# Kernel tuning notes

Hardware: AMD Instinct MI355X
Metric: run time of the kernel (lower is better)

The kernel has to match this reference:

```python
import jax, jax.numpy as jnp
import numpy as np

B, K1, N, DIMS = 512, 11, 5, 784  # K1 = K+1 samples per class incl. query
H = 512  # model_size


def _lstm(x_seq, W, U, b):
    """Keras-style LSTM, return_sequences=True.
    x_seq: [B, T, I]; W: [I, 4H]; U: [H, 4H]; b: [4H]. Gate order i,f,g,o.
    """
    units = U.shape[0]
    bsz = x_seq.shape[0]
    # precompute input projections for all timesteps: [T, B, 4H]
    xw = jnp.einsum('bti,ih->tbh', x_seq, W) + b

    def step(carry, xw_t):
        h, c = carry
        z = xw_t + h @ U  # [B, 4H]
        i, f, g, o = jnp.split(z, 4, axis=-1)
        i = jax.nn.sigmoid(i)
        f = jax.nn.sigmoid(f)
        g = jnp.tanh(g)
        o = jax.nn.sigmoid(o)
        c = f * c + i * g
        h = o * jnp.tanh(c)
        return (h, c), h

    init = (jnp.zeros((bsz, units), x_seq.dtype), jnp.zeros((bsz, units), x_seq.dtype))
    _, hs = jax.lax.scan(step, init, xw)  # hs: [T, B, H]
    return jnp.transpose(hs, (1, 0, 2))  # [B, T, H]


def setup_inputs() -> dict:
    key = jax.random.key(0)
    ks = jax.random.split(key, 8)
    return {
        'input_images': jax.random.normal(ks[0], (B, K1, N, DIMS), jnp.float32),
        'input_labels': jax.random.uniform(ks[1], (B, K1, N, N), jnp.float32),
        'W1': jax.random.normal(ks[2], (N + DIMS, 4 * H), jnp.float32) * 0.02,
        'U1': jax.random.normal(ks[3], (H, 4 * H), jnp.float32) * 0.02,
        'b1': jnp.zeros((4 * H,), jnp.float32),
        'W2': jax.random.normal(ks[4], (H, 4 * N), jnp.float32) * 0.02,
        'U2': jax.random.normal(ks[5], (N, 4 * N), jnp.float32) * 0.02,
        'b2': jnp.zeros((4 * N,), jnp.float32),
    }


def reference(input_images, input_labels, W1, U1, b1, W2, U2, b2):
    K = K1 - 1
    support_imgs = input_images[:, :K]               # [B, K, N, D]
    query_imgs = input_images[:, -1].reshape(-1, 1, N, DIMS)  # [B, 1, N, D]
    support_lbls = input_labels[:, :K]               # [B, K, N, N]
    concat_support = jnp.concatenate([support_imgs, support_lbls], axis=-1)
    zero_lbls = jnp.zeros((B, 1, N, N), input_images.dtype)
    concat_query = jnp.concatenate([query_imgs, zero_lbls], axis=-1)
    seq = jnp.concatenate([concat_support, concat_query], axis=1)  # [B, K1, N, N+D]
    seq = seq.reshape(-1, N * K1, N + DIMS)          # [B, T, N+D], T = N*K1
    x = _lstm(seq, W1, U1, b1)                       # [B, T, H]
    out = _lstm(x, W2, U2, b2)                       # [B, T, N]
    return out.reshape(-1, K1, N, N)
```

## Files before the change

### kernel.cpp

```cpp
#include <hip/hip_runtime.h>

typedef __attribute__((ext_vector_type(8))) __bf16 bf16x8;
typedef __attribute__((ext_vector_type(8))) unsigned short ushort8;
typedef __attribute__((ext_vector_type(4))) float f32x4;
typedef __attribute__((ext_vector_type(2))) unsigned long long u64x2;

#define DEVINL __device__ __forceinline__
#define RLX __ATOMIC_RELAXED
#define AGT __HIP_MEMORY_SCOPE_AGENT

constexpr int B_C    = 512;
constexpr int DIMS_C = 784;
constexpr int T_C    = 55;
constexpr int I0_C   = 789;
constexpr int KP_C   = 800;
constexpr int H_C    = 512;
constexpr int G4_C   = 2048;
constexpr int M1_C   = 28160;

constexpr size_t OFF_A    = 0;
constexpr size_t SZ_A     = (size_t)M1_C * KP_C * 2;
constexpr size_t OFF_W1T  = OFF_A + SZ_A;
constexpr size_t SZ_W1T   = (size_t)G4_C * KP_C * 2;
constexpr size_t OFF_U1T  = OFF_W1T + SZ_W1T;
constexpr size_t SZ_U1T   = (size_t)G4_C * H_C * 2;
constexpr size_t OFF_XW1  = OFF_U1T + SZ_U1T;
constexpr size_t SZ_XW1   = (size_t)M1_C * G4_C * 2;
constexpr size_t OFF_H    = OFF_XW1 + SZ_XW1;
constexpr size_t SZ_H     = (size_t)2 * B_C * H_C * 2;
constexpr size_t OFF_XMID = OFF_H + SZ_H;
constexpr size_t SZ_XMID  = (size_t)M1_C * H_C * 4;
constexpr size_t OFF_XW2  = OFF_XMID + SZ_XMID;
constexpr size_t SZ_XW2   = (size_t)M1_C * 20 * 4;
constexpr size_t OFF_W2T  = OFF_XW2 + SZ_XW2;
constexpr size_t SZ_W2T   = (size_t)20 * H_C * 4;
constexpr size_t OFF_CNT  = OFF_W2T + SZ_W2T;

DEVINL unsigned short f2bf(float f) {
  unsigned u = __builtin_bit_cast(unsigned, f);
  u += 0x7fffu + ((u >> 16) & 1u);
  return (unsigned short)(u >> 16);
}
DEVINL float sigm(float x) {
  return __builtin_amdgcn_rcpf(1.f + __builtin_amdgcn_exp2f(-1.4426950408889634f * x));
}
DEVINL float tanh_(float x) {
  return 2.f * __builtin_amdgcn_rcpf(1.f + __builtin_amdgcn_exp2f(-2.8853900817779268f * x)) - 1.f;
}
DEVINL void gl_lds16(const void* g, void* l) {
  __builtin_amdgcn_global_load_lds((const __attribute__((address_space(1))) void*)g,
                                   (__attribute__((address_space(3))) void*)l, 16, 0, 0);
}
DEVINL void gl_lds16_coh(const void* g, void* l) {
  __builtin_amdgcn_global_load_lds((const __attribute__((address_space(1))) void*)g,
                                   (__attribute__((address_space(3))) void*)l, 16, 0, 17);
}


__global__ void pack_a(const float* __restrict__ img, const float* __restrict__ lbl,
                       unsigned short* __restrict__ A) {
  int gid = blockIdx.x * blockDim.x + threadIdx.x;
  constexpr int CPR = KP_C / 8;
  if (gid >= M1_C * CPR) return;
  int r  = gid / CPR;
  int cc = gid - r * CPR;
  int t = r >> 9, b = r & 511;
  int k1 = t / 5, n = t - k1 * 5;
  int c0 = cc * 8;
  ushort8 v;
  if (c0 + 8 <= DIMS_C) {
    const float* p = img + ((size_t)((b * 11 + k1) * 5 + n)) * DIMS_C + c0;
    f32x4 x0 = *(const f32x4*)(p);
    f32x4 x1 = *(const f32x4*)(p + 4);
#pragma unroll
    for (int j = 0; j < 4; ++j) { v[j] = f2bf(x0[j]); v[4 + j] = f2bf(x1[j]); }
  } else {
#pragma unroll
    for (int j = 0; j < 8; ++j) {
      int c = c0 + j;
      float x = 0.f;
      if (c < DIMS_C) x = img[((size_t)((b * 11 + k1) * 5 + n)) * DIMS_C + c];
      else if (c < I0_C && k1 < 10) x = lbl[((size_t)((b * 11 + k1) * 5 + n)) * 5 + (c - DIMS_C)];
      v[j] = f2bf(x);
    }
  }
  *(ushort8*)(A + (size_t)r * KP_C + c0) = v;
}

__global__ void pack_w1t(const float* __restrict__ W1, unsigned short* __restrict__ W1T) {
  int gid = blockIdx.x * blockDim.x + threadIdx.x;
  if (gid >= G4_C * KP_C) return;
  int col = gid / KP_C, k = gid - col * KP_C;
  float x = (k < I0_C) ? W1[(size_t)k * G4_C + col] : 0.f;
  W1T[(size_t)col * KP_C + k] = f2bf(x);
}

__global__ void pack_u1t(const float* __restrict__ U1, unsigned short* __restrict__ U1T) {
  int gid = blockIdx.x * blockDim.x + threadIdx.x;
  if (gid >= G4_C * H_C) return;
  int col = gid / H_C, k = gid - col * H_C;
  U1T[(size_t)col * H_C + k] = f2bf(U1[(size_t)k * G4_C + col]);
}

__global__ void pack_w2t(const float* __restrict__ W2, float* __restrict__ W2T) {
  int gid = blockIdx.x * blockDim.x + threadIdx.x;
  if (gid >= 20 * H_C) return;
  int col = gid / H_C, k = gid - col * H_C;
  W2T[(size_t)col * H_C + k] = W2[(size_t)k * 20 + col];
}

__launch_bounds__(256, 2)
__global__ void gemm1(const unsigned short* __restrict__ A,
                      const unsigned short* __restrict__ Bt,
                      const float* __restrict__ bias,
                      _Float16* __restrict__ C)
{
  __shared__ unsigned short sA[2][128 * 32];
  __shared__ unsigned short sB[2][128 * 32];
  const int tid = threadIdx.x;
  const int w = tid >> 6, l = tid & 63;
  const int lo = l & 15, hi = l >> 4;
  const int wm = w >> 1, wn = w & 1;
  const int id = blockIdx.x;
  const int swz = (id & 7) * 440 + (id >> 3);
  const int by = swz >> 4;
  const int bx = swz & 15;

  const unsigned short* aSrc[2];
  const unsigned short* bSrc[2];
#pragma unroll
  for (int q = 0; q < 2; ++q) {
    int row = w * 32 + q * 16 + (l >> 2);
    int ch = l & 3;
    int sw = (row >> 1) & 3;
    aSrc[q] = A  + (size_t)(by * 128 + row) * KP_C + (ch ^ sw) * 8;
    bSrc[q] = Bt + (size_t)(bx * 128 + row) * KP_C + (ch ^ sw) * 8;
  }
  int aOff[4], bOff[4];
#pragma unroll
  for (int i = 0; i < 4; ++i) {
    int rA = wm * 64 + i * 16 + lo;
    aOff[i] = rA * 32 + ((hi ^ ((rA >> 1) & 3)) * 8);
    int rB = wn * 64 + i * 16 + lo;
    bOff[i] = rB * 32 + ((hi ^ ((rB >> 1) & 3)) * 8);
  }

  f32x4 acc[4][4];
#pragma unroll
  for (int i = 0; i < 4; ++i)
#pragma unroll
    for (int j = 0; j < 4; ++j) acc[i][j] = (f32x4){0.f, 0.f, 0.f, 0.f};

#define G1_STAGE(buf, ks)                                                  \
  {                                                                        \
    _Pragma("unroll")                                                      \
    for (int q = 0; q < 2; ++q) {                                          \
      gl_lds16(aSrc[q] + (ks) * 32, &sA[buf][w * 1024 + q * 512]);         \
      gl_lds16(bSrc[q] + (ks) * 32, &sB[buf][w * 1024 + q * 512]);         \
    }                                                                      \
  }

  G1_STAGE(0, 0);
  asm volatile("s_waitcnt vmcnt(0)" ::: "memory");
  __syncthreads();

  int cur = 0;
#pragma unroll 1
  for (int ks = 0; ks < KP_C / 32; ++ks) {
    if (ks < KP_C / 32 - 1) G1_STAGE(cur ^ 1, ks + 1);
    bf16x8 af[4], bfr[4];
#pragma unroll
    for (int i = 0; i < 4; ++i) {
      af[i]  = *(const bf16x8*)(&sA[cur][0] + aOff[i]);
      bfr[i] = *(const bf16x8*)(&sB[cur][0] + bOff[i]);
    }
#pragma unroll
    for (int mi = 0; mi < 4; ++mi)
#pragma unroll
      for (int ni = 0; ni < 4; ++ni)
        acc[mi][ni] = __builtin_amdgcn_mfma_f32_16x16x32_bf16(af[mi], bfr[ni], acc[mi][ni], 0, 0, 0);
    asm volatile("s_waitcnt vmcnt(0)" ::: "memory");
    __syncthreads();
    cur ^= 1;
  }
#undef G1_STAGE

  const size_t crow0 = (size_t)by * 128 + wm * 64;
  const int ccol0 = bx * 128 + wn * 64;
#pragma unroll
  for (int ni = 0; ni < 4; ++ni) {
    int col = ccol0 + ni * 16 + lo;
    float bv = bias[col];
#pragma unroll
    for (int mi = 0; mi < 4; ++mi) {
#pragma unroll
      for (int j = 0; j < 4; ++j) {
        size_t row = crow0 + mi * 16 + hi * 4 + j;
        C[row * G4_C + col] = (_Float16)(acc[mi][ni][j] + bv);
      }
    }
  }
}

__launch_bounds__(256, 2)
__global__ void lstm1(const _Float16* __restrict__ xw,
                      const unsigned short* __restrict__ U1T,
                      unsigned short* __restrict__ hbuf,
                      float* __restrict__ xmid,
                      unsigned int* __restrict__ cnt)
{
  __shared__ unsigned short sH[16 * 512];
  __shared__ float sG[4 * 16 * 32];

  const int tid = threadIdx.x;
  const int g = tid >> 6;
  const int l = tid & 63;
  const int lo = l & 15, hi = l >> 4;
  const int bg = blockIdx.x >> 4;
  const int cg = blockIdx.x & 15;
  const int brow0 = bg * 16;
  const int ub = cg * 32;

  bf16x8 bu[2][16];
#pragma unroll
  for (int nf = 0; nf < 2; ++nf) {
    const unsigned short* src = U1T + ((size_t)(g * H_C + ub + nf * 16 + lo)) * H_C + hi * 8;
#pragma unroll
    for (int kk = 0; kk < 16; ++kk)
      bu[nf][kk] = *(const bf16x8*)(src + kk * 32);
  }

  const int s0 = lo & 7;
  const int aO0 = lo * 1024;

  const int half = l >> 5;
  const int u = l & 31;
  const int rbase = g * 4 + half * 2;
  const int uread = u ^ (g << 3);

  float c_st[2] = {0.f, 0.f};

  const _Float16* xb = xw + (size_t)(brow0 + rbase) * G4_C + ub + u;
  float xwv[4][2];
#pragma unroll
  for (int g2 = 0; g2 < 4; ++g2)
#pragma unroll
    for (int j = 0; j < 2; ++j)
      xwv[g2][j] = (float)xb[(size_t)j * G4_C + g2 * H_C];

#pragma unroll 1
  for (int t = 0; t < T_C; ++t) {
    f32x4 acc[2];
    acc[0] = (f32x4){0.f, 0.f, 0.f, 0.f};
    acc[1] = (f32x4){0.f, 0.f, 0.f, 0.f};

    if (t > 0) {
      {
        const unsigned* fp = cnt + (size_t)(bg * 16 + (l & 15)) * 16;
        unsigned target = (unsigned)t;
        while (true) {
          unsigned v = __hip_atomic_load(fp, RLX, AGT);
          if (__all(v >= target)) break;
          __builtin_amdgcn_s_sleep(1);
        }
      }
      asm volatile("" ::: "memory");

      const unsigned short* hsrc = hbuf + (size_t)(t & 1) * (B_C * H_C);
#pragma unroll
      for (int p = 0; p < 4; ++p) {
        int row = g * 4 + p;
        gl_lds16_coh(hsrc + (size_t)(brow0 + row) * H_C + ((l ^ (row & 7)) * 8),
                     sH + row * 512);
      }
      asm volatile("s_waitcnt vmcnt(0)" ::: "memory");
      __syncthreads();

#pragma unroll
      for (int kk = 0; kk < 16; ++kk) {
        int off = (((kk * 4 + hi) ^ s0) << 4);
        bf16x8 a0 = *(const bf16x8*)((const char*)sH + aO0 + off);
        acc[0] = __builtin_amdgcn_mfma_f32_16x16x32_bf16(a0, bu[0][kk], acc[0], 0, 0, 0);
        acc[1] = __builtin_amdgcn_mfma_f32_16x16x32_bf16(a0, bu[1][kk], acc[1], 0, 0, 0);
      }
    }

#pragma unroll
    for (int nf = 0; nf < 2; ++nf)
#pragma unroll
      for (int j = 0; j < 4; ++j) {
        int row = hi * 4 + j;
        sG[g * 512 + row * 32 + ((nf * 16 + lo) ^ (hi << 3))] = acc[nf][j];
      }
    __syncthreads();

    float hnew[2];
#pragma unroll
    for (int j = 0; j < 2; ++j) {
      int r = rbase + j;
      float zi = sG[0 * 512 + r * 32 + uread] + xwv[0][j];
      float zf = sG[1 * 512 + r * 32 + uread] + xwv[1][j];
      float zg = sG[2 * 512 + r * 32 + uread] + xwv[2][j];
      float zo = sG[3 * 512 + r * 32 + uread] + xwv[3][j];
      float iv = sigm(zi), fv = sigm(zf), gv = tanh_(zg), ov = sigm(zo);
      float cv = fv * c_st[j] + iv * gv;
      c_st[j] = cv;
      hnew[j] = ov * tanh_(cv);
    }

    if (t < T_C - 1) {
      unsigned short* hd = hbuf + (size_t)((t & 1) ^ 1) * (B_C * H_C);
#pragma unroll
      for (int j = 0; j < 2; ++j) {
        float other = __shfl_xor(hnew[j], 1);
        if ((u & 1) == 0) {
          unsigned val = (unsigned)f2bf(hnew[j]) | ((unsigned)f2bf(other) << 16);
          __hip_atomic_store((unsigned*)(hd + (size_t)(brow0 + rbase + j) * H_C + ub + u), val,
                             RLX, AGT);
        }
      }

      __syncthreads();
      if (tid == 0)
        __hip_atomic_store(&cnt[(size_t)(bg * 16 + cg) * 16], (unsigned)(t + 1), RLX, AGT);

#pragma unroll
      for (int j = 0; j < 2; ++j)
        __builtin_nontemporal_store(hnew[j],
            &xmid[((size_t)t * B_C + brow0 + rbase + j) * H_C + ub + u]);
      const _Float16* xp = xb + (size_t)(t + 1) * B_C * G4_C;
#pragma unroll
      for (int g2 = 0; g2 < 4; ++g2)
#pragma unroll
        for (int j = 0; j < 2; ++j)
          xwv[g2][j] = (float)xp[(size_t)j * G4_C + g2 * H_C];
    } else {
#pragma unroll
      for (int j = 0; j < 2; ++j)
        __builtin_nontemporal_store(hnew[j],
            &xmid[((size_t)t * B_C + brow0 + rbase + j) * H_C + ub + u]);
    }
  }
}

__global__ void gemm2(const float* __restrict__ X,
                      const float* __restrict__ W2T,
                      const float* __restrict__ b2,
                      float* __restrict__ XW2)
{
  int r = blockIdx.x * blockDim.x + threadIdx.x;
  if (r >= M1_C) return;
  float acc[20];
#pragma unroll
  for (int j = 0; j < 20; ++j) acc[j] = b2[j];
  const float* xr = X + (size_t)r * H_C;
  for (int k = 0; k < H_C; k += 4) {
    f32x4 xv = *(const f32x4*)(xr + k);
#pragma unroll
    for (int j = 0; j < 20; ++j) {
      f32x4 wv = *(const f32x4*)(W2T + (size_t)j * H_C + k);
      acc[j] += xv[0]*wv[0] + xv[1]*wv[1] + xv[2]*wv[2] + xv[3]*wv[3];
    }
  }
  float* op = XW2 + (size_t)r * 20;
#pragma unroll
  for (int j = 0; j < 20; ++j) op[j] = acc[j];
}

__global__ void lstm2(const float* __restrict__ XW2,
                      const float* __restrict__ U2,
                      float* __restrict__ out)
{
  int b = blockIdx.x * blockDim.x + threadIdx.x;
  if (b >= B_C) return;
  float u2[5][20];
#pragma unroll
  for (int k = 0; k < 5; ++k)
#pragma unroll
    for (int j = 0; j < 20; ++j) u2[k][j] = U2[k * 20 + j];
  float h[5] = {0, 0, 0, 0, 0}, c[5] = {0, 0, 0, 0, 0};
  for (int t = 0; t < T_C; ++t) {
    const float* xr = XW2 + ((size_t)t * B_C + b) * 20;
    float z[20];
#pragma unroll
    for (int j = 0; j < 20; ++j) z[j] = xr[j];
#pragma unroll
    for (int k = 0; k < 5; ++k) {
      float hk = h[k];
#pragma unroll
      for (int j = 0; j < 20; ++j) z[j] += hk * u2[k][j];
    }
#pragma unroll
    for (int n = 0; n < 5; ++n) {
      float iv = sigm(z[n]), fv = sigm(z[5 + n]), gv = tanh_(z[10 + n]), ov = sigm(z[15 + n]);
      c[n] = fv * c[n] + iv * gv;
      h[n] = ov * tanh_(c[n]);
    }
    int k1 = t / 5, nn = t - k1 * 5;
    float* op = out + (((size_t)b * 11 + k1) * 5 + nn) * 5;
#pragma unroll
    for (int j = 0; j < 5; ++j) op[j] = h[j];
  }
}

extern "C" void kernel_launch(void* const* d_in, const int* in_sizes, int n_in,
                              void* d_out, int out_size, void* d_ws, size_t ws_size,
                              hipStream_t stream) {
  (void)in_sizes; (void)n_in; (void)out_size; (void)ws_size;
  const float* img = (const float*)d_in[0];
  const float* lbl = (const float*)d_in[1];
  const float* W1  = (const float*)d_in[2];
  const float* U1  = (const float*)d_in[3];
  const float* b1  = (const float*)d_in[4];
  const float* W2  = (const float*)d_in[5];
  const float* U2  = (const float*)d_in[6];
  const float* b2  = (const float*)d_in[7];

  char* ws = (char*)d_ws;
  unsigned short* A    = (unsigned short*)(ws + OFF_A);
  unsigned short* W1T  = (unsigned short*)(ws + OFF_W1T);
  unsigned short* U1T  = (unsigned short*)(ws + OFF_U1T);
  _Float16*       XW1  = (_Float16*)      (ws + OFF_XW1);
  unsigned short* HB   = (unsigned short*)(ws + OFF_H);
  float*          XMID = (float*)         (ws + OFF_XMID);
  float*          XW2  = (float*)         (ws + OFF_XW2);
  float*          W2T  = (float*)         (ws + OFF_W2T);
  unsigned int*   CNT  = (unsigned int*)  (ws + OFF_CNT);

  hipMemsetAsync(CNT, 0, 512 * 64, stream);

  pack_a  <<<(M1_C * (KP_C / 8)) / 256, 256, 0, stream>>>(img, lbl, A);
  pack_w1t<<<(G4_C * KP_C) / 256,      256, 0, stream>>>(W1, W1T);
  pack_u1t<<<(G4_C * H_C) / 256,       256, 0, stream>>>(U1, U1T);
  pack_w2t<<<(20 * H_C + 255) / 256,   256, 0, stream>>>(W2, W2T);

  gemm1<<<3520, 256, 0, stream>>>(A, W1T, b1, XW1);
  lstm1<<<512, 256, 0, stream>>>(XW1, U1T, HB, XMID, CNT);
  gemm2<<<(M1_C + 255) / 256, 256, 0, stream>>>(XMID, W2T, b2, XW2);
  lstm2<<<8, 64, 0, stream>>>(XW2, U2, (float*)d_out);
}
```

Measured before the change: 458.2 us.

## Split LSTM1 across twice the blocks, parallelize gemm2 outputs, prefetch lstm2 inputs

The persistent recurrent kernel lstm1 now uses 1024 blocks, each owning 16 hidden units instead of 32. Each wave issues one MFMA chain instead of two, cutting register pressure so launch bounds allow 4 blocks per CU; each thread also handles a single (row, unit) pair. The cost is that every block now waits on 32 producer flags instead of 16 and reloads the same h tile, which doubles the redundant h reads. Separately, gemm2 splits each row's 20 outputs across 4 threads for more parallelism, and lstm2 prefetches the next timestep's input projection into registers to hide load latency.

```diff
diff --git a/kernel.cpp b/kernel.cpp
--- a/kernel.cpp
+++ b/kernel.cpp
@@ -202,7 +202,7 @@
   }
 }
 
-__launch_bounds__(256, 2)
+__launch_bounds__(256, 4)
 __global__ void lstm1(const _Float16* __restrict__ xw,
                       const unsigned short* __restrict__ U1T,
                       unsigned short* __restrict__ hbuf,
@@ -210,53 +210,46 @@
                       unsigned int* __restrict__ cnt)
 {
   __shared__ unsigned short sH[16 * 512];
-  __shared__ float sG[4 * 16 * 32];
+  __shared__ float sG[4 * 16 * 16];
 
   const int tid = threadIdx.x;
   const int g = tid >> 6;
   const int l = tid & 63;
   const int lo = l & 15, hi = l >> 4;
-  const int bg = blockIdx.x >> 4;
-  const int cg = blockIdx.x & 15;
+  const int bg = blockIdx.x >> 5;
+  const int cg = blockIdx.x & 31;
   const int brow0 = bg * 16;
-  const int ub = cg * 32;
-
-  bf16x8 bu[2][16];
-#pragma unroll
-  for (int nf = 0; nf < 2; ++nf) {
-    const unsigned short* src = U1T + ((size_t)(g * H_C + ub + nf * 16 + lo)) * H_C + hi * 8;
+  const int ub = cg * 16;
+
+  bf16x8 bu[16];
+  {
+    const unsigned short* src = U1T + ((size_t)(g * H_C + ub + lo)) * H_C + hi * 8;
 #pragma unroll
     for (int kk = 0; kk < 16; ++kk)
-      bu[nf][kk] = *(const bf16x8*)(src + kk * 32);
+      bu[kk] = *(const bf16x8*)(src + kk * 32);
   }
 
   const int s0 = lo & 7;
   const int aO0 = lo * 1024;
 
-  const int half = l >> 5;
-  const int u = l & 31;
-  const int rbase = g * 4 + half * 2;
-  const int uread = u ^ (g << 3);
-
-  float c_st[2] = {0.f, 0.f};
-
-  const _Float16* xb = xw + (size_t)(brow0 + rbase) * G4_C + ub + u;
-  float xwv[4][2];
+  const int r = tid >> 4;
+  const int u = tid & 15;
+
+  float c_st = 0.f;
+
+  const _Float16* xb = xw + (size_t)(brow0 + r) * G4_C + ub + u;
+  float xwv[4];
 #pragma unroll
   for (int g2 = 0; g2 < 4; ++g2)
-#pragma unroll
-    for (int j = 0; j < 2; ++j)
-      xwv[g2][j] = (float)xb[(size_t)j * G4_C + g2 * H_C];
+    xwv[g2] = (float)xb[g2 * H_C];
 
 #pragma unroll 1
   for (int t = 0; t < T_C; ++t) {
-    f32x4 acc[2];
-    acc[0] = (f32x4){0.f, 0.f, 0.f, 0.f};
-    acc[1] = (f32x4){0.f, 0.f, 0.f, 0.f};
+    f32x4 acc = (f32x4){0.f, 0.f, 0.f, 0.f};
 
     if (t > 0) {
       {
-        const unsigned* fp = cnt + (size_t)(bg * 16 + (l & 15)) * 16;
+        const unsigned* fp = cnt + (size_t)(bg * 32 + (l & 31)) * 16;
         unsigned target = (unsigned)t;
         while (true) {
           unsigned v = __hip_atomic_load(fp, RLX, AGT);
@@ -280,65 +273,48 @@
       for (int kk = 0; kk < 16; ++kk) {
         int off = (((kk * 4 + hi) ^ s0) << 4);
         bf16x8 a0 = *(const bf16x8*)((const char*)sH + aO0 + off);
-        acc[0] = __builtin_amdgcn_mfma_f32_16x16x32_bf16(a0, bu[0][kk], acc[0], 0, 0, 0);
-        acc[1] = __builtin_amdgcn_mfma_f32_16x16x32_bf16(a0, bu[1][kk], acc[1], 0, 0, 0);
+        acc = __builtin_amdgcn_mfma_f32_16x16x32_bf16(a0, bu[kk], acc, 0, 0, 0);
       }
     }
 
 #pragma unroll
-    for (int nf = 0; nf < 2; ++nf)
-#pragma unroll
-      for (int j = 0; j < 4; ++j) {
-        int row = hi * 4 + j;
-        sG[g * 512 + row * 32 + ((nf * 16 + lo) ^ (hi << 3))] = acc[nf][j];
-      }
+    for (int j = 0; j < 4; ++j)
+      sG[g * 256 + (hi * 4 + j) * 16 + lo] = acc[j];
     __syncthreads();
 
-    float hnew[2];
-#pragma unroll
-    for (int j = 0; j < 2; ++j) {
-      int r = rbase + j;
-      float zi = sG[0 * 512 + r * 32 + uread] + xwv[0][j];
-      float zf = sG[1 * 512 + r * 32 + uread] + xwv[1][j];
-      float zg = sG[2 * 512 + r * 32 + uread] + xwv[2][j];
-      float zo = sG[3 * 512 + r * 32 + uread] + xwv[3][j];
-      float iv = sigm(zi), fv = sigm(zf), gv = tanh_(zg), ov = sigm(zo);
-      float cv = fv * c_st[j] + iv * gv;
-      c_st[j] = cv;
-      hnew[j] = ov * tanh_(cv);
-    }
+    float zi = sG[0 * 256 + r * 16 + u] + xwv[0];
+    float zf = sG[1 * 256 + r * 16 + u] + xwv[1];
+    float zg = sG[2 * 256 + r * 16 + u] + xwv[2];
+    float zo = sG[3 * 256 + r * 16 + u] + xwv[3];
+    float iv = sigm(zi), fv = sigm(zf), gv = tanh_(zg), ov = sigm(zo);
+    float cv = fv * c_st + iv * gv;
+    c_st = cv;
+    float hnew = ov * tanh_(cv);
 
     if (t < T_C - 1) {
       unsigned short* hd = hbuf + (size_t)((t & 1) ^ 1) * (B_C * H_C);
-#pragma unroll
-      for (int j = 0; j < 2; ++j) {
-        float other = __shfl_xor(hnew[j], 1);
+      {
+        float other = __shfl_xor(hnew, 1);
         if ((u & 1) == 0) {
-          unsigned val = (unsigned)f2bf(hnew[j]) | ((unsigned)f2bf(other) << 16);
-          __hip_atomic_store((unsigned*)(hd + (size_t)(brow0 + rbase + j) * H_C + ub + u), val,
+          unsigned val = (unsigned)f2bf(hnew) | ((unsigned)f2bf(other) << 16);
+          __hip_atomic_store((unsigned*)(hd + (size_t)(brow0 + r) * H_C + ub + u), val,
                              RLX, AGT);
         }
       }
 
       __syncthreads();
       if (tid == 0)
-        __hip_atomic_store(&cnt[(size_t)(bg * 16 + cg) * 16], (unsigned)(t + 1), RLX, AGT);
-
-#pragma unroll
-      for (int j = 0; j < 2; ++j)
-        __builtin_nontemporal_store(hnew[j],
-            &xmid[((size_t)t * B_C + brow0 + rbase + j) * H_C + ub + u]);
+        __hip_atomic_store(&cnt[(size_t)(bg * 32 + cg) * 16], (unsigned)(t + 1), RLX, AGT);
+
+      __builtin_nontemporal_store(hnew,
+          &xmid[((size_t)t * B_C + brow0 + r) * H_C + ub + u]);
       const _Float16* xp = xb + (size_t)(t + 1) * B_C * G4_C;
 #pragma unroll
       for (int g2 = 0; g2 < 4; ++g2)
-#pragma unroll
-        for (int j = 0; j < 2; ++j)
-          xwv[g2][j] = (float)xp[(size_t)j * G4_C + g2 * H_C];
+        xwv[g2] = (float)xp[g2 * H_C];
     } else {
-#pragma unroll
-      for (int j = 0; j < 2; ++j)
-        __builtin_nontemporal_store(hnew[j],
-            &xmid[((size_t)t * B_C + brow0 + rbase + j) * H_C + ub + u]);
+      __builtin_nontemporal_store(hnew,
+          &xmid[((size_t)t * B_C + brow0 + r) * H_C + ub + u]);
     }
   }
 }
@@ -348,23 +324,24 @@
                       const float* __restrict__ b2,
                       float* __restrict__ XW2)
 {
-  int r = blockIdx.x * blockDim.x + threadIdx.x;
-  if (r >= M1_C) return;
-  float acc[20];
-#pragma unroll
-  for (int j = 0; j < 20; ++j) acc[j] = b2[j];
+  int gid = blockIdx.x * blockDim.x + threadIdx.x;
+  if (gid >= M1_C * 4) return;
+  int r = gid >> 2, jq = gid & 3;
   const float* xr = X + (size_t)r * H_C;
+  float acc[5];
+#pragma unroll
+  for (int jj = 0; jj < 5; ++jj) acc[jj] = b2[jq * 5 + jj];
   for (int k = 0; k < H_C; k += 4) {
     f32x4 xv = *(const f32x4*)(xr + k);
 #pragma unroll
-    for (int j = 0; j < 20; ++j) {
-      f32x4 wv = *(const f32x4*)(W2T + (size_t)j * H_C + k);
-      acc[j] += xv[0]*wv[0] + xv[1]*wv[1] + xv[2]*wv[2] + xv[3]*wv[3];
-    }
-  }
-  float* op = XW2 + (size_t)r * 20;
-#pragma unroll
-  for (int j = 0; j < 20; ++j) op[j] = acc[j];
+    for (int jj = 0; jj < 5; ++jj) {
+      f32x4 wv = *(const f32x4*)(W2T + (size_t)(jq * 5 + jj) * H_C + k);
+      acc[jj] += xv[0]*wv[0] + xv[1]*wv[1] + xv[2]*wv[2] + xv[3]*wv[3];
+    }
+  }
+  float* op = XW2 + (size_t)r * 20 + jq * 5;
+#pragma unroll
+  for (int jj = 0; jj < 5; ++jj) op[jj] = acc[jj];
 }
 
 __global__ void lstm2(const float* __restrict__ XW2,
@@ -379,11 +356,24 @@
 #pragma unroll
     for (int j = 0; j < 20; ++j) u2[k][j] = U2[k * 20 + j];
   float h[5] = {0, 0, 0, 0, 0}, c[5] = {0, 0, 0, 0, 0};
+
+  float zbuf[20];
+  {
+    const float* xr = XW2 + (size_t)b * 20;
+#pragma unroll
+    for (int j = 0; j < 20; ++j) zbuf[j] = xr[j];
+  }
+
+#pragma unroll 1
   for (int t = 0; t < T_C; ++t) {
-    const float* xr = XW2 + ((size_t)t * B_C + b) * 20;
     float z[20];
 #pragma unroll
-    for (int j = 0; j < 20; ++j) z[j] = xr[j];
+    for (int j = 0; j < 20; ++j) z[j] = zbuf[j];
+    if (t < T_C - 1) {
+      const float* xn = XW2 + ((size_t)(t + 1) * B_C + b) * 20;
+#pragma unroll
+      for (int j = 0; j < 20; ++j) zbuf[j] = xn[j];
+    }
 #pragma unroll
     for (int k = 0; k < 5; ++k) {
       float hk = h[k];
@@ -427,7 +417,7 @@
   float*          W2T  = (float*)         (ws + OFF_W2T);
   unsigned int*   CNT  = (unsigned int*)  (ws + OFF_CNT);
 
-  hipMemsetAsync(CNT, 0, 512 * 64, stream);
+  hipMemsetAsync(CNT, 0, 1024 * 64, stream);
 
   pack_a  <<<(M1_C * (KP_C / 8)) / 256, 256, 0, stream>>>(img, lbl, A);
   pack_w1t<<<(G4_C * KP_C) / 256,      256, 0, stream>>>(W1, W1T);
@@ -435,7 +425,7 @@
   pack_w2t<<<(20 * H_C + 255) / 256,   256, 0, stream>>>(W2, W2T);
 
   gemm1<<<3520, 256, 0, stream>>>(A, W1T, b1, XW1);
-  lstm1<<<512, 256, 0, stream>>>(XW1, U1T, HB, XMID, CNT);
-  gemm2<<<(M1_C + 255) / 256, 256, 0, stream>>>(XMID, W2T, b2, XW2);
+  lstm1<<<1024, 256, 0, stream>>>(XW1, U1T, HB, XMID, CNT);
+  gemm2<<<(M1_C * 4 + 255) / 256, 256, 0, stream>>>(XMID, W2T, b2, XW2);
   lstm2<<<8, 64, 0, stream>>>(XW2, U2, (float*)d_out);
 }
```

Measured after the change: 598.8 us. 30.7% more time.
